# Kernel optimization log

Measured on AMD Instinct MI355X. Metric: run time of the kernel, lower is better.

The kernel has to match this reference:

```python
import jax, jax.numpy as jnp
import numpy as np

D_MODEL = 256
NHEAD = 8
HEAD_DIM = D_MODEL // NHEAD
NLAYERS = 8
LAYER_NAMES = ('self', 'cross', 'self', 'cross', 'self', 'cross', 'self', 'cross')
LN_EPS = 1e-5
ATTN_EPS = 1e-6


def _layernorm(x, g, b):
    mu = jnp.mean(x, axis=-1, keepdims=True)
    var = jnp.mean(jnp.square(x - mu), axis=-1, keepdims=True)
    return (x - mu) * jax.lax.rsqrt(var + LN_EPS) * g + b


def _encoder_layer(x, source, Wq, Wk, Wv, Wm, W1, W2, g1, b1, g2, b2):
    # x: [N, L, C], source: [N, S, C]; weights stored [in, out] so y = x @ W
    bs, L, C = x.shape
    S = source.shape[1]
    q = (x @ Wq).reshape(bs, L, NHEAD, HEAD_DIM)
    k = (source @ Wk).reshape(bs, S, NHEAD, HEAD_DIM)
    v = (source @ Wv).reshape(bs, S, NHEAD, HEAD_DIM)
    # LoFTR LinearAttention: feature map elu(x)+1, O(N d^2) kernelized attention
    Q = jax.nn.elu(q) + 1.0
    K = jax.nn.elu(k) + 1.0
    v_n = v / S  # normalize values by kv length for numerical stability
    KV = jnp.einsum('nshd,nshv->nhdv', K, v_n)            # [N,H,D,D]
    Z = 1.0 / (jnp.einsum('nlhd,nhd->nlh', Q, K.sum(axis=1)) + ATTN_EPS)
    msg = jnp.einsum('nlhd,nhdv,nlh->nlhv', Q, KV, Z) * S  # [N,L,H,D]
    msg = msg.reshape(bs, L, C) @ Wm
    msg = _layernorm(msg, g1, b1)
    h = jnp.concatenate([x, msg], axis=-1)                 # [N,L,2C]
    h = jax.nn.relu(h @ W1) @ W2
    h = _layernorm(h, g2, b2)
    return x + h


def _transformer(feat0, feat1, Wq, Wk, Wv, Wm, W1, W2, g1, b1, g2, b2):
    for i, name in enumerate(LAYER_NAMES):
        p = (Wq[i], Wk[i], Wv[i], Wm[i], W1[i], W2[i], g1[i], b1[i], g2[i], b2[i])
        if name == 'self':
            feat0 = _encoder_layer(feat0, feat0, *p)
            feat1 = _encoder_layer(feat1, feat1, *p)
        else:  # cross
            new0 = _encoder_layer(feat0, feat1, *p)
            feat1 = _encoder_layer(feat1, feat0, *p)
            feat0 = new0
    return feat0, feat1


def setup_inputs() -> dict:
    key = jax.random.key(0)
    ks = jax.random.split(key, 8)
    N, L = 4, 4800
    feat0 = jax.random.normal(ks[0], (N, L, D_MODEL), jnp.float32)
    feat1 = jax.random.normal(ks[1], (N, L, D_MODEL), jnp.float32)
    xav = lambda k, fi, fo: jax.random.normal(k, (NLAYERS, fi, fo), jnp.float32) * float(np.sqrt(2.0 / (fi + fo)))
    Wq = xav(ks[2], D_MODEL, D_MODEL)
    Wk = xav(ks[3], D_MODEL, D_MODEL)
    Wv = xav(ks[4], D_MODEL, D_MODEL)
    Wm = xav(ks[5], D_MODEL, D_MODEL)
    W1 = xav(ks[6], 2 * D_MODEL, 2 * D_MODEL)
    W2 = xav(ks[7], 2 * D_MODEL, D_MODEL)
    g1 = jnp.ones((NLAYERS, D_MODEL), jnp.float32)
    b1 = jnp.zeros((NLAYERS, D_MODEL), jnp.float32)
    g2 = jnp.ones((NLAYERS, D_MODEL), jnp.float32)
    b2 = jnp.zeros((NLAYERS, D_MODEL), jnp.float32)
    return dict(feat0=feat0, feat1=feat1, Wq=Wq, Wk=Wk, Wv=Wv, Wm=Wm,
                W1=W1, W2=W2, g1=g1, b1=b1, g2=g2, b2=b2)


def reference(feat0, feat1, Wq, Wk, Wv, Wm, W1, W2, g1, b1, g2, b2):
    return _transformer(feat0, feat1, Wq, Wk, Wv, Wm, W1, W2, g1, b1, g2, b2)
```

## Files before the change

kernel.cpp:

```cpp
#include <hip/hip_runtime.h>
#include <math.h>

#define RTOT 19200
#define RALL 38400
#define CDIM 256
#define SLEN 4800
#define NB 8
#define NHEAD 8
#define HDIM 32
#define SEG 25
#define SCHUNK 192

typedef __attribute__((ext_vector_type(8))) short short8v;
typedef __attribute__((ext_vector_type(4))) float f32x4;

__device__ __forceinline__ ushort f2b(float f) {
    unsigned u = __float_as_uint(f);
    unsigned r = (u + 0x7FFFu + ((u >> 16) & 1u)) >> 16;
    return (ushort)r;
}
__device__ __forceinline__ float b2f(ushort u) {
    return __uint_as_float(((unsigned)u) << 16);
}

template<int ACT> __device__ __forceinline__ float actf(float v) {
    if (ACT == 1) return v > 0.0f ? v + 1.0f : __expf(v);
    if (ACT == 2) return v > 0.0f ? v : 0.0f;
    return v;
}

__device__ __forceinline__ void gload16(const void* g, void* l) {
    __builtin_amdgcn_global_load_lds((const __attribute__((address_space(1))) void*)g,
                                     (__attribute__((address_space(3))) void*)l, 16, 0, 0);
}

template<int ACT, bool CONCAT, int OMODE>
__global__ __launch_bounds__(256) void gemm_bf16(
    const ushort* __restrict__ A, const ushort* __restrict__ A2, int lda,
    const ushort* __restrict__ Bt,
    ushort* __restrict__ O0, ushort* __restrict__ O1, ushort* __restrict__ O2,
    int N, int K)
{
    __shared__ __align__(16) ushort As[128 * 32];
    __shared__ __align__(16) ushort Bs[128 * 32];
    const int t = threadIdx.x;
    const int wave = t >> 6, lane = t & 63;
    const int bm = blockIdx.y * 128, bn = blockIdx.x * 128;
    const int wr = wave >> 1, wc = wave & 1;
    const int lr = lane & 15, lk = (lane >> 4) * 8;

    const int srow = t >> 2;
    const int sgrp = ((t & 3) * 8) ^ ((srow & 3) * 8);
    const ushort* bAr = A + (size_t)(bm + srow) * lda + sgrp;
    const ushort* bA2r = CONCAT ? (A2 + (size_t)(bm + srow) * lda + sgrp) : (const ushort*)0;
    const ushort* bBr = Bt + (size_t)(bn + srow) * K + sgrp;
    char* ldsA = (char*)As + wave * 1024;
    char* ldsB = (char*)Bs + wave * 1024;
    const size_t a64 = (size_t)64 * lda;
    const size_t b64 = (size_t)64 * K;

    const f32x4 z4 = {0.f, 0.f, 0.f, 0.f};
    f32x4 acc[4][4];
    #pragma unroll
    for (int m = 0; m < 4; ++m)
        #pragma unroll
        for (int n = 0; n < 4; ++n) acc[m][n] = z4;

    for (int k0 = 0; k0 < K; k0 += 32) {
        const ushort* ga;
        if (CONCAT) ga = (k0 < 256) ? (bAr + k0) : (bA2r + (k0 - 256));
        else        ga = bAr + k0;
        gload16(ga, ldsA);
        gload16(ga + a64, ldsA + 4096);
        gload16(bBr + k0, ldsB);
        gload16(bBr + k0 + b64, ldsB + 4096);
        __syncthreads();

        short8v af[4], bfr[4];
        #pragma unroll
        for (int m = 0; m < 4; ++m) {
            const int r = wr * 64 + m * 16 + lr;
            af[m] = *(const short8v*)&As[r * 32 + (lk ^ ((r & 3) * 8))];
        }
        #pragma unroll
        for (int n = 0; n < 4; ++n) {
            const int r = wc * 64 + n * 16 + lr;
            bfr[n] = *(const short8v*)&Bs[r * 32 + (lk ^ ((r & 3) * 8))];
        }
        #pragma unroll
        for (int m = 0; m < 4; ++m)
            #pragma unroll
            for (int n = 0; n < 4; ++n)
                acc[m][n] = __builtin_amdgcn_mfma_f32_16x16x32_bf16(af[m], bfr[n], acc[m][n], 0, 0, 0);
        __syncthreads();
    }

    const int orow = bm + wr * 64 + (lane >> 4) * 4;
    const int ocol = bn + wc * 64 + lr;
    #pragma unroll
    for (int m = 0; m < 4; ++m)
        #pragma unroll
        for (int n = 0; n < 4; ++n)
            #pragma unroll
            for (int j = 0; j < 4; ++j) {
                const float v = acc[m][n][j];
                const size_t row = (size_t)(orow + m * 16 + j);
                const int col = ocol + n * 16;
                if (OMODE == 0) {
                    O0[row * N + col] = f2b(actf<ACT>(v));
                } else {
                    const int seg = col >> 8, c = col & 255;
                    ushort* dst = seg == 0 ? O0 : (seg == 1 ? O1 : O2);
                    dst[row * 256 + c] = f2b(seg < 2 ? actf<1>(v) : v);
                }
            }
}

__global__ __launch_bounds__(256) void gemm_ln32(
    const ushort* __restrict__ A, int lda,
    const ushort* __restrict__ Bt,
    const float* __restrict__ g, const float* __restrict__ bb,
    const float* __restrict__ rx0, const float* __restrict__ rx1,
    float* __restrict__ outf, ushort* __restrict__ outb, int K)
{
    __shared__ __align__(16) ushort As[32 * 32];
    __shared__ __align__(16) ushort Bs[256 * 32];
    __shared__ float red[2][4][32];
    const int t = threadIdx.x;
    const int wave = t >> 6, lane = t & 63;
    const int bm = blockIdx.x * 32;
    const int lr = lane & 15, kg = lane >> 4, lk = kg * 8;

    const int srow = t >> 2;
    const int sg = ((t & 3) * 8) ^ ((srow & 3) * 8);
    const ushort* aP = A + (size_t)(bm + srow) * lda + sg;
    const ushort* bP = Bt + (size_t)srow * K + sg;
    char* ldsA = (char*)As + wave * 1024;
    char* ldsB = (char*)Bs + wave * 1024;
    const size_t b64 = (size_t)64 * K;

    const f32x4 z4 = {0.f, 0.f, 0.f, 0.f};
    f32x4 acc[2][4];
    #pragma unroll
    for (int m = 0; m < 2; ++m)
        #pragma unroll
        for (int n = 0; n < 4; ++n) acc[m][n] = z4;

    for (int k0 = 0; k0 < K; k0 += 32) {
        if (srow < 32) gload16(aP + k0, ldsA);
        gload16(bP + k0, ldsB);
        gload16(bP + k0 + b64, ldsB + 4096);
        gload16(bP + k0 + 2 * b64, ldsB + 8192);
        gload16(bP + k0 + 3 * b64, ldsB + 12288);
        __syncthreads();

        short8v af[2], bfr[4];
        #pragma unroll
        for (int m = 0; m < 2; ++m) {
            const int r = m * 16 + lr;
            af[m] = *(const short8v*)&As[r * 32 + (lk ^ ((r & 3) * 8))];
        }
        #pragma unroll
        for (int n = 0; n < 4; ++n) {
            const int r = wave * 64 + n * 16 + lr;
            bfr[n] = *(const short8v*)&Bs[r * 32 + (lk ^ ((r & 3) * 8))];
        }
        #pragma unroll
        for (int m = 0; m < 2; ++m)
            #pragma unroll
            for (int n = 0; n < 4; ++n)
                acc[m][n] = __builtin_amdgcn_mfma_f32_16x16x32_bf16(af[m], bfr[n], acc[m][n], 0, 0, 0);
        __syncthreads();
    }

    #pragma unroll
    for (int m = 0; m < 2; ++m)
        #pragma unroll
        for (int j = 0; j < 4; ++j) {
            float s = 0.f, q = 0.f;
            #pragma unroll
            for (int n = 0; n < 4; ++n) { const float v = acc[m][n][j]; s += v; q += v * v; }
            #pragma unroll
            for (int mk = 1; mk < 16; mk <<= 1) { s += __shfl_xor(s, mk); q += __shfl_xor(q, mk); }
            if (lr == 0) {
                red[0][wave][m * 16 + kg * 4 + j] = s;
                red[1][wave][m * 16 + kg * 4 + j] = q;
            }
        }
    __syncthreads();

    float gv[4], bv[4];
    #pragma unroll
    for (int n = 0; n < 4; ++n) {
        const int col = wave * 64 + n * 16 + lr;
        gv[n] = g[col]; bv[n] = bb[col];
    }
    const float* rxb = (bm < RTOT) ? rx0 + (size_t)bm * CDIM : rx1 + (size_t)(bm - RTOT) * CDIM;

    #pragma unroll
    for (int m = 0; m < 2; ++m)
        #pragma unroll
        for (int j = 0; j < 4; ++j) {
            const int row = m * 16 + kg * 4 + j;
            const float tot = red[0][0][row] + red[0][1][row] + red[0][2][row] + red[0][3][row];
            const float tq  = red[1][0][row] + red[1][1][row] + red[1][2][row] + red[1][3][row];
            const float mu = tot * (1.0f / 256.0f);
            const float var = tq * (1.0f / 256.0f) - mu * mu;
            const float inv = rsqrtf(var + 1e-5f);
            const size_t go = (size_t)(bm + row) * CDIM;
            #pragma unroll
            for (int n = 0; n < 4; ++n) {
                const int col = wave * 64 + n * 16 + lr;
                float val = (acc[m][n][j] - mu) * inv * gv[n] + bv[n];
                val += rxb[(size_t)row * CDIM + col];
                outf[go + col] = val;
                outb[go + col] = f2b(val);
            }
        }
}

__global__ __launch_bounds__(256) void attn_wm_ln(
    const ushort* __restrict__ Qb, const ushort* __restrict__ KVbT,
    const ushort* __restrict__ Ksb, const ushort* __restrict__ WmT,
    const float* __restrict__ g, const float* __restrict__ bb,
    ushort* __restrict__ mln, int xorv)
{
    __shared__ __align__(16) ushort Ms[32 * 256];
    __shared__ __align__(16) ushort Bs[256 * 32];
    __shared__ float red[2][4][32];
    const int t = threadIdx.x, wave = t >> 6, lane = t & 63;
    const int bm = blockIdx.x * 32;
    const int n = bm / SLEN, src = n ^ xorv;
    const int lr = lane & 15, kg = lane >> 4, lk = kg * 8;
    const f32x4 z4 = {0.f, 0.f, 0.f, 0.f};

    if (wave < 2) {
        const int rw = wave * 16;
        const size_t qrow = ((size_t)bm + rw + lr) * CDIM;
        char* mb = (char*)Ms;
        #pragma unroll
        for (int h = 0; h < NHEAD; ++h) {
            const short8v af = *(const short8v*)&Qb[qrow + h * 32 + kg * 8];
            const ushort* bbp = KVbT + ((size_t)(src * NHEAD + h)) * 1024;
            const short8v b0 = *(const short8v*)&bbp[lr * 32 + kg * 8];
            const short8v b1 = *(const short8v*)&bbp[(16 + lr) * 32 + kg * 8];
            const short8v bz = *(const short8v*)&Ksb[((size_t)(src * NHEAD + h)) * 512 + lr * 32 + kg * 8];
            f32x4 a0 = __builtin_amdgcn_mfma_f32_16x16x32_bf16(af, b0, z4, 0, 0, 0);
            f32x4 a1 = __builtin_amdgcn_mfma_f32_16x16x32_bf16(af, b1, z4, 0, 0, 0);
            f32x4 az = __builtin_amdgcn_mfma_f32_16x16x32_bf16(af, bz, z4, 0, 0, 0);
            #pragma unroll
            for (int j = 0; j < 4; ++j) {
                const float zj = __shfl(az[j], lane & 48);
                const float rz = 1.0f / (zj + 1e-6f);
                const int orow = rw + kg * 4 + j;
                const int swz = (orow & 7) << 4;
                *(ushort*)(mb + ((orow * 512 + (h * 32 + lr) * 2) ^ swz)) = f2b(a0[j] * rz);
                *(ushort*)(mb + ((orow * 512 + (h * 32 + 16 + lr) * 2) ^ swz)) = f2b(a1[j] * rz);
            }
        }
    }
    __syncthreads();

    const int srow = t >> 2;
    const int sg = ((t & 3) * 8) ^ ((srow & 3) * 8);
    const ushort* bP = WmT + (size_t)srow * 256 + sg;
    char* ldsB = (char*)Bs + wave * 1024;

    f32x4 acc[2][4];
    #pragma unroll
    for (int m = 0; m < 2; ++m)
        #pragma unroll
        for (int nn = 0; nn < 4; ++nn) acc[m][nn] = z4;

    for (int k0 = 0; k0 < 256; k0 += 32) {
        gload16(bP + k0, ldsB);
        gload16(bP + k0 + 64 * 256, ldsB + 4096);
        gload16(bP + k0 + 128 * 256, ldsB + 8192);
        gload16(bP + k0 + 192 * 256, ldsB + 12288);
        __syncthreads();

        short8v af[2], bfr[4];
        #pragma unroll
        for (int m = 0; m < 2; ++m) {
            const int r = m * 16 + lr;
            af[m] = *(const short8v*)((char*)Ms + ((r * 512 + k0 * 2 + kg * 16) ^ ((r & 7) << 4)));
        }
        #pragma unroll
        for (int nn = 0; nn < 4; ++nn) {
            const int r = wave * 64 + nn * 16 + lr;
            bfr[nn] = *(const short8v*)&Bs[r * 32 + (lk ^ ((r & 3) * 8))];
        }
        #pragma unroll
        for (int m = 0; m < 2; ++m)
            #pragma unroll
            for (int nn = 0; nn < 4; ++nn)
                acc[m][nn] = __builtin_amdgcn_mfma_f32_16x16x32_bf16(af[m], bfr[nn], acc[m][nn], 0, 0, 0);
        __syncthreads();
    }

    #pragma unroll
    for (int m = 0; m < 2; ++m)
        #pragma unroll
        for (int j = 0; j < 4; ++j) {
            float s = 0.f, q = 0.f;
            #pragma unroll
            for (int nn = 0; nn < 4; ++nn) { const float v = acc[m][nn][j]; s += v; q += v * v; }
            #pragma unroll
            for (int mk = 1; mk < 16; mk <<= 1) { s += __shfl_xor(s, mk); q += __shfl_xor(q, mk); }
            if (lr == 0) {
                red[0][wave][m * 16 + kg * 4 + j] = s;
                red[1][wave][m * 16 + kg * 4 + j] = q;
            }
        }
    __syncthreads();

    float gv[4], bv[4];
    #pragma unroll
    for (int nn = 0; nn < 4; ++nn) {
        const int col = wave * 64 + nn * 16 + lr;
        gv[nn] = g[col]; bv[nn] = bb[col];
    }
    #pragma unroll
    for (int m = 0; m < 2; ++m)
        #pragma unroll
        for (int j = 0; j < 4; ++j) {
            const int row = m * 16 + kg * 4 + j;
            const float tot = red[0][0][row] + red[0][1][row] + red[0][2][row] + red[0][3][row];
            const float tq  = red[1][0][row] + red[1][1][row] + red[1][2][row] + red[1][3][row];
            const float mu = tot * (1.0f / 256.0f);
            const float var = tq * (1.0f / 256.0f) - mu * mu;
            const float inv = rsqrtf(var + 1e-5f);
            const size_t go = (size_t)(bm + row) * CDIM;
            #pragma unroll
            for (int nn = 0; nn < 4; ++nn) {
                const int col = wave * 64 + nn * 16 + lr;
                mln[go + col] = f2b((acc[m][nn][j] - mu) * inv * gv[nn] + bv[nn]);
            }
        }
}

__global__ __launch_bounds__(256) void wconv_t(
    const float* __restrict__ src, ushort* __restrict__ dst, int R, int C, size_t dstride)
{
    __shared__ float tile[32][33];
    const int l = blockIdx.z;
    const int r0 = blockIdx.y * 32, c0 = blockIdx.x * 32;
    const int tx = threadIdx.x & 31, ty = threadIdx.x >> 5;
    const float* s = src + (size_t)l * R * C;
    ushort* d = dst + (size_t)l * dstride;
    for (int i = ty; i < 32; i += 8) tile[i][tx] = s[(size_t)(r0 + i) * C + c0 + tx];
    __syncthreads();
    for (int i = ty; i < 32; i += 8) d[(size_t)(c0 + i) * R + r0 + tx] = f2b(tile[tx][i]);
}

__global__ __launch_bounds__(256) void kv_part_k(
    const ushort* __restrict__ Kb, const ushort* __restrict__ Vb,
    float* __restrict__ KVp, float* __restrict__ Ksp)
{
    const int blk = blockIdx.x;
    const int seg = blk % SEG;
    const int h = (blk / SEG) % NHEAD;
    const int n = blk / (SEG * NHEAD);
    const int s0 = seg * SCHUNK;
    __shared__ float Ks[16][32];
    __shared__ float Vs[16][32];
    const int t = threadIdx.x;
    const int rr = t >> 4, c2 = (t & 15) * 2;
    const int d = t >> 3, v0 = (t & 7) * 4;
    float a0 = 0, a1 = 0, a2 = 0, a3 = 0, ksum = 0;
    for (int c = 0; c < SCHUNK; c += 16) {
        const size_t off = ((size_t)(n * SLEN + s0 + c + rr)) * CDIM + h * HDIM + c2;
        const ushort2 ku = *(const ushort2*)&Kb[off];
        const ushort2 vu = *(const ushort2*)&Vb[off];
        Ks[rr][c2] = b2f(ku.x); Ks[rr][c2 + 1] = b2f(ku.y);
        Vs[rr][c2] = b2f(vu.x); Vs[rr][c2 + 1] = b2f(vu.y);
        __syncthreads();
        #pragma unroll
        for (int q = 0; q < 16; ++q) {
            const float kd = Ks[q][d];
            a0 += kd * Vs[q][v0 + 0];
            a1 += kd * Vs[q][v0 + 1];
            a2 += kd * Vs[q][v0 + 2];
            a3 += kd * Vs[q][v0 + 3];
        }
        if (t < 32) {
            #pragma unroll
            for (int q = 0; q < 16; ++q) ksum += Ks[q][t];
        }
        __syncthreads();
    }
    float* kvp = KVp + ((size_t)((n * NHEAD + h) * SEG + seg)) * 1024;
    kvp[t * 4 + 0] = a0;
    kvp[t * 4 + 1] = a1;
    kvp[t * 4 + 2] = a2;
    kvp[t * 4 + 3] = a3;
    if (t < 32) Ksp[((size_t)((n * NHEAD + h) * SEG + seg)) * 32 + t] = ksum;
}

__global__ __launch_bounds__(256) void kv_reduce_k(
    const float* __restrict__ KVp, const float* __restrict__ Ksp,
    ushort* __restrict__ KVbT, ushort* __restrict__ Ksb)
{
    const int nh = blockIdx.x;
    const int t = threadIdx.x;
    #pragma unroll
    for (int i = 0; i < 4; ++i) {
        const int idx = t * 4 + i;
        const int v = idx >> 5, d = idx & 31;
        float s = 0;
        for (int seg = 0; seg < SEG; ++seg)
            s += KVp[((size_t)(nh * SEG + seg)) * 1024 + d * 32 + v];
        KVbT[(size_t)nh * 1024 + idx] = f2b(s);
    }
    #pragma unroll
    for (int i = 0; i < 2; ++i) {
        const int idx = t * 2 + i;
        const int c = idx >> 5, d = idx & 31;
        float s = 0;
        if (c == 0)
            for (int seg = 0; seg < SEG; ++seg)
                s += Ksp[((size_t)(nh * SEG + seg)) * 32 + d];
        Ksb[(size_t)nh * 512 + idx] = f2b(s);
    }
}

__global__ __launch_bounds__(256) void cvt_in_k(const float* __restrict__ src, ushort* __restrict__ dst) {
    const size_t i = ((size_t)blockIdx.x * 256 + threadIdx.x) * 4;
    const float4 v = *(const float4*)&src[i];
    ushort4 ob = make_ushort4(f2b(v.x), f2b(v.y), f2b(v.z), f2b(v.w));
    *(ushort4*)&dst[i] = ob;
}

struct Ws {
    float *xf, *KVp, *Ksp;
    ushort *xb, *Qb, *Kb, *Vb, *h1b, *KVbT, *Ksb;
    ushort *WqkvT, *WmT, *W1T, *W2T;
};

static void layer_pass(const float* rx0, const float* rx1, float* destf, int xorv,
                       const ushort* WqkvT, const ushort* WmT,
                       const ushort* W1T, const ushort* W2T,
                       const float* g1, const float* b1,
                       const float* g2, const float* b2,
                       const Ws& w, hipStream_t stream)
{
    const dim3 blk(256);
    gemm_bf16<0, false, 1><<<dim3(6, RALL / 128), blk, 0, stream>>>(
        w.xb, nullptr, 256, WqkvT, w.Qb, w.Kb, w.Vb, 768, 256);
    kv_part_k<<<dim3(NB * NHEAD * SEG), blk, 0, stream>>>(w.Kb, w.Vb, w.KVp, w.Ksp);
    kv_reduce_k<<<dim3(NB * NHEAD), blk, 0, stream>>>(w.KVp, w.Ksp, w.KVbT, w.Ksb);
    attn_wm_ln<<<dim3(RALL / 32), blk, 0, stream>>>(
        w.Qb, w.KVbT, w.Ksb, WmT, g1, b1, w.Kb, xorv);
    gemm_bf16<2, true, 0><<<dim3(4, RALL / 128), blk, 0, stream>>>(
        w.xb, w.Kb, 256, W1T, w.h1b, nullptr, nullptr, 512, 512);
    gemm_ln32<<<dim3(RALL / 32), blk, 0, stream>>>(
        w.h1b, 512, W2T, g2, b2, rx0, rx1, destf, w.xb, 512);
}

extern "C" void kernel_launch(void* const* d_in, const int* in_sizes, int n_in,
                              void* d_out, int out_size, void* d_ws, size_t ws_size,
                              hipStream_t stream) {
    (void)in_sizes; (void)n_in; (void)out_size; (void)ws_size;
    const float* f0in = (const float*)d_in[0];
    const float* f1in = (const float*)d_in[1];
    const float* WqA = (const float*)d_in[2];
    const float* WkA = (const float*)d_in[3];
    const float* WvA = (const float*)d_in[4];
    const float* WmA = (const float*)d_in[5];
    const float* W1A = (const float*)d_in[6];
    const float* W2A = (const float*)d_in[7];
    const float* g1A = (const float*)d_in[8];
    const float* b1A = (const float*)d_in[9];
    const float* g2A = (const float*)d_in[10];
    const float* b2A = (const float*)d_in[11];

    float* outf = (float*)d_out;
    const size_t RC = (size_t)RTOT * CDIM;
    const size_t RAC = (size_t)RALL * CDIM;

    float* wsf = (float*)d_ws;
    Ws w;
    w.xf  = wsf;
    w.KVp = w.xf + RAC;
    w.Ksp = w.KVp + (size_t)64 * SEG * 1024;
    ushort* p = (ushort*)(w.Ksp + 64 * SEG * 32);
    w.xb = p;   p += RAC;
    w.Qb = p;   p += RAC;
    w.Kb = p;   p += RAC;
    w.Vb = p;   p += RAC;
    w.h1b = p;  p += (size_t)RALL * 512;
    w.KVbT = p; p += 64 * 1024;
    w.Ksb = p;  p += 64 * 512;
    w.WqkvT = p; p += (size_t)8 * 768 * 256;
    w.WmT = p;  p += (size_t)8 * 256 * 256;
    w.W1T = p;  p += (size_t)8 * 512 * 512;
    w.W2T = p;  p += (size_t)8 * 512 * 256;

    const dim3 blk(256);
    wconv_t<<<dim3(8, 8, 8), blk, 0, stream>>>(WqA, w.WqkvT,             256, 256, 768 * 256);
    wconv_t<<<dim3(8, 8, 8), blk, 0, stream>>>(WkA, w.WqkvT + 256 * 256, 256, 256, 768 * 256);
    wconv_t<<<dim3(8, 8, 8), blk, 0, stream>>>(WvA, w.WqkvT + 512 * 256, 256, 256, 768 * 256);
    wconv_t<<<dim3(8, 8, 8), blk, 0, stream>>>(WmA, w.WmT, 256, 256, 65536);
    wconv_t<<<dim3(16, 16, 8), blk, 0, stream>>>(W1A, w.W1T, 512, 512, 262144);
    wconv_t<<<dim3(8, 16, 8), blk, 0, stream>>>(W2A, w.W2T, 512, 256, 131072);

    cvt_in_k<<<dim3(RC / 1024), blk, 0, stream>>>(f0in, w.xb);
    cvt_in_k<<<dim3(RC / 1024), blk, 0, stream>>>(f1in, w.xb + RC);

    for (int l = 0; l < 8; ++l) {
        const int xorv = (l & 1) ? 4 : 0;
        const float* rx0 = (l == 0) ? f0in : w.xf;
        const float* rx1 = (l == 0) ? f1in : w.xf + RC;
        float* destf = (l == 7) ? outf : w.xf;
        layer_pass(rx0, rx1, destf, xorv,
                   w.WqkvT + (size_t)l * 768 * 256,
                   w.WmT + (size_t)l * 65536,
                   w.W1T + (size_t)l * 262144,
                   w.W2T + (size_t)l * 131072,
                   g1A + l * 256, b1A + l * 256, g2A + l * 256, b2A + l * 256,
                   w, stream);
    }
}
```

Before: 1.501 ms.

## Fuse MLP GEMMs with LayerNorm and double-buffer weight tiles

Replaces the separate W1 GEMM (with concat and ReLU) and the W2+LayerNorm kernel with a single mlp_ln kernel. It keeps the concatenated 32x512 input tile and each 128-wide chunk of the hidden activation in LDS, so the h1b intermediate is never written to or read back from global memory. The QKV GEMM and the Wm-projection kernel now double-buffer their LDS weight tiles so global loads overlap the MFMA work. The attention-message step is also spread across all four waves. In exchange, every 32-row block streams the full W1 and W2 weights, and the larger LDS footprint may lower occupancy.

```diff
diff --git a/kernel.cpp b/kernel.cpp
--- a/kernel.cpp
+++ b/kernel.cpp
@@ -7,7 +7,6 @@
 #define SLEN 4800
 #define NB 8
 #define NHEAD 8
-#define HDIM 32
 #define SEG 25
 #define SCHUNK 192
 
@@ -23,26 +22,19 @@
     return __uint_as_float(((unsigned)u) << 16);
 }
 
-template<int ACT> __device__ __forceinline__ float actf(float v) {
-    if (ACT == 1) return v > 0.0f ? v + 1.0f : __expf(v);
-    if (ACT == 2) return v > 0.0f ? v : 0.0f;
-    return v;
-}
+__device__ __forceinline__ float elu1(float v) { return v > 0.0f ? v + 1.0f : __expf(v); }
 
 __device__ __forceinline__ void gload16(const void* g, void* l) {
     __builtin_amdgcn_global_load_lds((const __attribute__((address_space(1))) void*)g,
                                      (__attribute__((address_space(3))) void*)l, 16, 0, 0);
 }
 
-template<int ACT, bool CONCAT, int OMODE>
-__global__ __launch_bounds__(256) void gemm_bf16(
-    const ushort* __restrict__ A, const ushort* __restrict__ A2, int lda,
-    const ushort* __restrict__ Bt,
-    ushort* __restrict__ O0, ushort* __restrict__ O1, ushort* __restrict__ O2,
-    int N, int K)
-{
-    __shared__ __align__(16) ushort As[128 * 32];
-    __shared__ __align__(16) ushort Bs[128 * 32];
+__global__ __launch_bounds__(256) void qkv_gemm(
+    const ushort* __restrict__ A, const ushort* __restrict__ Bt,
+    ushort* __restrict__ Oq, ushort* __restrict__ Ok, ushort* __restrict__ Ov)
+{
+    __shared__ __align__(16) ushort As[2][128 * 32];
+    __shared__ __align__(16) ushort Bs[2][128 * 32];
     const int t = threadIdx.x;
     const int wave = t >> 6, lane = t & 63;
     const int bm = blockIdx.y * 128, bn = blockIdx.x * 128;
@@ -51,13 +43,8 @@
 
     const int srow = t >> 2;
     const int sgrp = ((t & 3) * 8) ^ ((srow & 3) * 8);
-    const ushort* bAr = A + (size_t)(bm + srow) * lda + sgrp;
-    const ushort* bA2r = CONCAT ? (A2 + (size_t)(bm + srow) * lda + sgrp) : (const ushort*)0;
-    const ushort* bBr = Bt + (size_t)(bn + srow) * K + sgrp;
-    char* ldsA = (char*)As + wave * 1024;
-    char* ldsB = (char*)Bs + wave * 1024;
-    const size_t a64 = (size_t)64 * lda;
-    const size_t b64 = (size_t)64 * K;
+    const ushort* bAr = A + (size_t)(bm + srow) * 256 + sgrp;
+    const ushort* bBr = Bt + (size_t)(bn + srow) * 256 + sgrp;
 
     const f32x4 z4 = {0.f, 0.f, 0.f, 0.f};
     f32x4 acc[4][4];
@@ -66,26 +53,30 @@
         #pragma unroll
         for (int n = 0; n < 4; ++n) acc[m][n] = z4;
 
-    for (int k0 = 0; k0 < K; k0 += 32) {
-        const ushort* ga;
-        if (CONCAT) ga = (k0 < 256) ? (bAr + k0) : (bA2r + (k0 - 256));
-        else        ga = bAr + k0;
-        gload16(ga, ldsA);
-        gload16(ga + a64, ldsA + 4096);
-        gload16(bBr + k0, ldsB);
-        gload16(bBr + k0 + b64, ldsB + 4096);
-        __syncthreads();
-
+    auto stage = [&](int k0, int b) {
+        char* la = (char*)As[b] + wave * 1024;
+        char* lb = (char*)Bs[b] + wave * 1024;
+        gload16(bAr + k0, la);
+        gload16(bAr + k0 + 64 * 256, la + 4096);
+        gload16(bBr + k0, lb);
+        gload16(bBr + k0 + 64 * 256, lb + 4096);
+    };
+
+    stage(0, 0);
+    __syncthreads();
+    int cur = 0;
+    for (int k0 = 0; k0 < 256; k0 += 32) {
+        if (k0 + 32 < 256) stage(k0 + 32, cur ^ 1);
         short8v af[4], bfr[4];
         #pragma unroll
         for (int m = 0; m < 4; ++m) {
             const int r = wr * 64 + m * 16 + lr;
-            af[m] = *(const short8v*)&As[r * 32 + (lk ^ ((r & 3) * 8))];
+            af[m] = *(const short8v*)&As[cur][r * 32 + (lk ^ ((r & 3) * 8))];
         }
         #pragma unroll
         for (int n = 0; n < 4; ++n) {
             const int r = wc * 64 + n * 16 + lr;
-            bfr[n] = *(const short8v*)&Bs[r * 32 + (lk ^ ((r & 3) * 8))];
+            bfr[n] = *(const short8v*)&Bs[cur][r * 32 + (lk ^ ((r & 3) * 8))];
         }
         #pragma unroll
         for (int m = 0; m < 4; ++m)
@@ -93,6 +84,7 @@
             for (int n = 0; n < 4; ++n)
                 acc[m][n] = __builtin_amdgcn_mfma_f32_16x16x32_bf16(af[m], bfr[n], acc[m][n], 0, 0, 0);
         __syncthreads();
+        cur ^= 1;
     }
 
     const int orow = bm + wr * 64 + (lane >> 4) * 4;
@@ -106,71 +98,92 @@
                 const float v = acc[m][n][j];
                 const size_t row = (size_t)(orow + m * 16 + j);
                 const int col = ocol + n * 16;
-                if (OMODE == 0) {
-                    O0[row * N + col] = f2b(actf<ACT>(v));
-                } else {
-                    const int seg = col >> 8, c = col & 255;
-                    ushort* dst = seg == 0 ? O0 : (seg == 1 ? O1 : O2);
-                    dst[row * 256 + c] = f2b(seg < 2 ? actf<1>(v) : v);
-                }
-            }
-}
-
-__global__ __launch_bounds__(256) void gemm_ln32(
-    const ushort* __restrict__ A, int lda,
-    const ushort* __restrict__ Bt,
+                const int seg = col >> 8, c = col & 255;
+                ushort* dst = seg == 0 ? Oq : (seg == 1 ? Ok : Ov);
+                dst[row * 256 + c] = f2b(seg < 2 ? elu1(v) : v);
+            }
+}
+
+__global__ __launch_bounds__(256) void attn_wm_ln(
+    const ushort* __restrict__ Qb, const ushort* __restrict__ KVbT,
+    const ushort* __restrict__ Ksb, const ushort* __restrict__ WmT,
     const float* __restrict__ g, const float* __restrict__ bb,
-    const float* __restrict__ rx0, const float* __restrict__ rx1,
-    float* __restrict__ outf, ushort* __restrict__ outb, int K)
-{
-    __shared__ __align__(16) ushort As[32 * 32];
-    __shared__ __align__(16) ushort Bs[256 * 32];
+    ushort* __restrict__ mln, int xorv)
+{
+    __shared__ __align__(16) ushort Ms[32 * 256];
+    __shared__ __align__(16) ushort Bs[2][256 * 32];
     __shared__ float red[2][4][32];
-    const int t = threadIdx.x;
-    const int wave = t >> 6, lane = t & 63;
+    const int t = threadIdx.x, wave = t >> 6, lane = t & 63;
     const int bm = blockIdx.x * 32;
+    const int n = bm / SLEN, src = n ^ xorv;
     const int lr = lane & 15, kg = lane >> 4, lk = kg * 8;
+    const f32x4 z4 = {0.f, 0.f, 0.f, 0.f};
 
     const int srow = t >> 2;
     const int sg = ((t & 3) * 8) ^ ((srow & 3) * 8);
-    const ushort* aP = A + (size_t)(bm + srow) * lda + sg;
-    const ushort* bP = Bt + (size_t)srow * K + sg;
-    char* ldsA = (char*)As + wave * 1024;
-    char* ldsB = (char*)Bs + wave * 1024;
-    const size_t b64 = (size_t)64 * K;
-
-    const f32x4 z4 = {0.f, 0.f, 0.f, 0.f};
+    const ushort* bP = WmT + (size_t)srow * 256 + sg;
+    auto stageB = [&](int k0, int b) {
+        char* lb = (char*)Bs[b] + wave * 1024;
+        gload16(bP + k0, lb);
+        gload16(bP + k0 + 64 * 256, lb + 4096);
+        gload16(bP + k0 + 128 * 256, lb + 8192);
+        gload16(bP + k0 + 192 * 256, lb + 12288);
+    };
+    stageB(0, 0);
+
+    {
+        const int rw = (wave & 1) * 16;
+        const size_t qrow = ((size_t)bm + rw + lr) * CDIM;
+        char* mb = (char*)Ms;
+        for (int h = (wave >> 1); h < NHEAD; h += 2) {
+            const short8v af = *(const short8v*)&Qb[qrow + h * 32 + kg * 8];
+            const ushort* bbp = KVbT + ((size_t)(src * NHEAD + h)) * 1024;
+            const short8v b0 = *(const short8v*)&bbp[lr * 32 + kg * 8];
+            const short8v b1 = *(const short8v*)&bbp[(16 + lr) * 32 + kg * 8];
+            const short8v bz = *(const short8v*)&Ksb[((size_t)(src * NHEAD + h)) * 512 + lr * 32 + kg * 8];
+            f32x4 a0 = __builtin_amdgcn_mfma_f32_16x16x32_bf16(af, b0, z4, 0, 0, 0);
+            f32x4 a1 = __builtin_amdgcn_mfma_f32_16x16x32_bf16(af, b1, z4, 0, 0, 0);
+            f32x4 az = __builtin_amdgcn_mfma_f32_16x16x32_bf16(af, bz, z4, 0, 0, 0);
+            #pragma unroll
+            for (int j = 0; j < 4; ++j) {
+                const float zj = __shfl(az[j], lane & 48);
+                const float rz = 1.0f / (zj + 1e-6f);
+                const int orow = rw + kg * 4 + j;
+                const int swz = (orow & 7) << 4;
+                *(ushort*)(mb + ((orow * 512 + (h * 32 + lr) * 2) ^ swz)) = f2b(a0[j] * rz);
+                *(ushort*)(mb + ((orow * 512 + (h * 32 + 16 + lr) * 2) ^ swz)) = f2b(a1[j] * rz);
+            }
+        }
+    }
+    __syncthreads();
+
     f32x4 acc[2][4];
     #pragma unroll
     for (int m = 0; m < 2; ++m)
         #pragma unroll
-        for (int n = 0; n < 4; ++n) acc[m][n] = z4;
-
-    for (int k0 = 0; k0 < K; k0 += 32) {
-        if (srow < 32) gload16(aP + k0, ldsA);
-        gload16(bP + k0, ldsB);
-        gload16(bP + k0 + b64, ldsB + 4096);
-        gload16(bP + k0 + 2 * b64, ldsB + 8192);
-        gload16(bP + k0 + 3 * b64, ldsB + 12288);
-        __syncthreads();
-
+        for (int nn = 0; nn < 4; ++nn) acc[m][nn] = z4;
+
+    int cur = 0;
+    for (int k0 = 0; k0 < 256; k0 += 32) {
+        if (k0 + 32 < 256) stageB(k0 + 32, cur ^ 1);
         short8v af[2], bfr[4];
         #pragma unroll
         for (int m = 0; m < 2; ++m) {
             const int r = m * 16 + lr;
-            af[m] = *(const short8v*)&As[r * 32 + (lk ^ ((r & 3) * 8))];
-        }
-        #pragma unroll
-        for (int n = 0; n < 4; ++n) {
-            const int r = wave * 64 + n * 16 + lr;
-            bfr[n] = *(const short8v*)&Bs[r * 32 + (lk ^ ((r & 3) * 8))];
+            af[m] = *(const short8v*)((char*)Ms + ((r * 512 + k0 * 2 + kg * 16) ^ ((r & 7) << 4)));
+        }
+        #pragma unroll
+        for (int nn = 0; nn < 4; ++nn) {
+            const int r = wave * 64 + nn * 16 + lr;
+            bfr[nn] = *(const short8v*)&Bs[cur][r * 32 + (lk ^ ((r & 3) * 8))];
         }
         #pragma unroll
         for (int m = 0; m < 2; ++m)
             #pragma unroll
-            for (int n = 0; n < 4; ++n)
-                acc[m][n] = __builtin_amdgcn_mfma_f32_16x16x32_bf16(af[m], bfr[n], acc[m][n], 0, 0, 0);
+            for (int nn = 0; nn < 4; ++nn)
+                acc[m][nn] = __builtin_amdgcn_mfma_f32_16x16x32_bf16(af[m], bfr[nn], acc[m][nn], 0, 0, 0);
         __syncthreads();
+        cur ^= 1;
     }
 
     #pragma unroll
@@ -179,7 +192,7 @@
         for (int j = 0; j < 4; ++j) {
             float s = 0.f, q = 0.f;
             #pragma unroll
-            for (int n = 0; n < 4; ++n) { const float v = acc[m][n][j]; s += v; q += v * v; }
+            for (int nn = 0; nn < 4; ++nn) { const float v = acc[m][nn][j]; s += v; q += v * v; }
             #pragma unroll
             for (int mk = 1; mk < 16; mk <<= 1) { s += __shfl_xor(s, mk); q += __shfl_xor(q, mk); }
             if (lr == 0) {
@@ -191,12 +204,10 @@
 
     float gv[4], bv[4];
     #pragma unroll
-    for (int n = 0; n < 4; ++n) {
-        const int col = wave * 64 + n * 16 + lr;
-        gv[n] = g[col]; bv[n] = bb[col];
-    }
-    const float* rxb = (bm < RTOT) ? rx0 + (size_t)bm * CDIM : rx1 + (size_t)(bm - RTOT) * CDIM;
-
+    for (int nn = 0; nn < 4; ++nn) {
+        const int col = wave * 64 + nn * 16 + lr;
+        gv[nn] = g[col]; bv[nn] = bb[col];
+    }
     #pragma unroll
     for (int m = 0; m < 2; ++m)
         #pragma unroll
@@ -209,93 +220,141 @@
             const float inv = rsqrtf(var + 1e-5f);
             const size_t go = (size_t)(bm + row) * CDIM;
             #pragma unroll
-            for (int n = 0; n < 4; ++n) {
-                const int col = wave * 64 + n * 16 + lr;
-                float val = (acc[m][n][j] - mu) * inv * gv[n] + bv[n];
-                val += rxb[(size_t)row * CDIM + col];
-                outf[go + col] = val;
-                outb[go + col] = f2b(val);
-            }
-        }
-}
-
-__global__ __launch_bounds__(256) void attn_wm_ln(
-    const ushort* __restrict__ Qb, const ushort* __restrict__ KVbT,
-    const ushort* __restrict__ Ksb, const ushort* __restrict__ WmT,
+            for (int nn = 0; nn < 4; ++nn) {
+                const int col = wave * 64 + nn * 16 + lr;
+                mln[go + col] = f2b((acc[m][nn][j] - mu) * inv * gv[nn] + bv[nn]);
+            }
+        }
+}
+
+__global__ __launch_bounds__(256) void mlp_ln(
+    const ushort* __restrict__ xb, const ushort* __restrict__ mlnSrc,
+    const ushort* __restrict__ W1T, const ushort* __restrict__ W2T,
     const float* __restrict__ g, const float* __restrict__ bb,
-    ushort* __restrict__ mln, int xorv)
-{
-    __shared__ __align__(16) ushort Ms[32 * 256];
-    __shared__ __align__(16) ushort Bs[256 * 32];
+    const float* __restrict__ rx0, const float* __restrict__ rx1,
+    float* __restrict__ outf, ushort* __restrict__ outb)
+{
+    __shared__ __align__(16) ushort A512[32 * 512];
+    __shared__ __align__(16) ushort Bs[2][256 * 32];
+    __shared__ __align__(16) ushort H1[32 * 128];
     __shared__ float red[2][4][32];
     const int t = threadIdx.x, wave = t >> 6, lane = t & 63;
     const int bm = blockIdx.x * 32;
-    const int n = bm / SLEN, src = n ^ xorv;
     const int lr = lane & 15, kg = lane >> 4, lk = kg * 8;
     const f32x4 z4 = {0.f, 0.f, 0.f, 0.f};
 
-    if (wave < 2) {
-        const int rw = wave * 16;
-        const size_t qrow = ((size_t)bm + rw + lr) * CDIM;
-        char* mb = (char*)Ms;
-        #pragma unroll
-        for (int h = 0; h < NHEAD; ++h) {
-            const short8v af = *(const short8v*)&Qb[qrow + h * 32 + kg * 8];
-            const ushort* bbp = KVbT + ((size_t)(src * NHEAD + h)) * 1024;
-            const short8v b0 = *(const short8v*)&bbp[lr * 32 + kg * 8];
-            const short8v b1 = *(const short8v*)&bbp[(16 + lr) * 32 + kg * 8];
-            const short8v bz = *(const short8v*)&Ksb[((size_t)(src * NHEAD + h)) * 512 + lr * 32 + kg * 8];
-            f32x4 a0 = __builtin_amdgcn_mfma_f32_16x16x32_bf16(af, b0, z4, 0, 0, 0);
-            f32x4 a1 = __builtin_amdgcn_mfma_f32_16x16x32_bf16(af, b1, z4, 0, 0, 0);
-            f32x4 az = __builtin_amdgcn_mfma_f32_16x16x32_bf16(af, bz, z4, 0, 0, 0);
-            #pragma unroll
-            for (int j = 0; j < 4; ++j) {
-                const float zj = __shfl(az[j], lane & 48);
-                const float rz = 1.0f / (zj + 1e-6f);
-                const int orow = rw + kg * 4 + j;
-                const int swz = (orow & 7) << 4;
-                *(ushort*)(mb + ((orow * 512 + (h * 32 + lr) * 2) ^ swz)) = f2b(a0[j] * rz);
-                *(ushort*)(mb + ((orow * 512 + (h * 32 + 16 + lr) * 2) ^ swz)) = f2b(a1[j] * rz);
-            }
-        }
-    }
-    __syncthreads();
+    {
+        const ushort* mln2 = mlnSrc - 256;
+        #pragma unroll
+        for (int i = 0; i < 8; ++i) {
+            const int row = i * 4 + wave;
+            const int gl = lane ^ (row & 7);
+            const ushort* s = (gl < 32) ? (xb + (size_t)(bm + row) * 256 + gl * 8)
+                                        : (mln2 + (size_t)(bm + row) * 256 + gl * 8);
+            gload16(s, (char*)A512 + row * 1024);
+        }
+    }
 
     const int srow = t >> 2;
     const int sg = ((t & 3) * 8) ^ ((srow & 3) * 8);
-    const ushort* bP = WmT + (size_t)srow * 256 + sg;
-    char* ldsB = (char*)Bs + wave * 1024;
-
-    f32x4 acc[2][4];
+    auto stageIdx = [&](int idx, int b) {
+        char* lb = (char*)Bs[b] + wave * 1024;
+        const int c = idx / 12, s = idx % 12;
+        if (s < 8) {
+            const ushort* p = W1T + (size_t)(c * 128 + srow) * 512 + s * 64 + sg;
+            gload16(p, lb);
+            gload16(p + (size_t)64 * 512, lb + 4096);
+            gload16(p + 32, lb + 8192);
+            gload16(p + (size_t)64 * 512 + 32, lb + 12288);
+        } else {
+            const ushort* p = W2T + (size_t)srow * 512 + c * 128 + (s - 8) * 32 + sg;
+            gload16(p, lb);
+            gload16(p + (size_t)64 * 512, lb + 4096);
+            gload16(p + (size_t)128 * 512, lb + 8192);
+            gload16(p + (size_t)192 * 512, lb + 12288);
+        }
+    };
+
+    f32x4 acc2[2][4];
     #pragma unroll
     for (int m = 0; m < 2; ++m)
         #pragma unroll
-        for (int nn = 0; nn < 4; ++nn) acc[m][nn] = z4;
-
-    for (int k0 = 0; k0 < 256; k0 += 32) {
-        gload16(bP + k0, ldsB);
-        gload16(bP + k0 + 64 * 256, ldsB + 4096);
-        gload16(bP + k0 + 128 * 256, ldsB + 8192);
-        gload16(bP + k0 + 192 * 256, ldsB + 12288);
+        for (int nn = 0; nn < 4; ++nn) acc2[m][nn] = z4;
+
+    stageIdx(0, 0);
+    __syncthreads();
+    int cur = 0, sid = 0;
+
+    for (int c = 0; c < 4; ++c) {
+        f32x4 acc1[2][2];
+        #pragma unroll
+        for (int m = 0; m < 2; ++m)
+            #pragma unroll
+            for (int nn = 0; nn < 2; ++nn) acc1[m][nn] = z4;
+
+        for (int s = 0; s < 8; ++s) {
+            if (sid + 1 < 48) stageIdx(sid + 1, cur ^ 1);
+            #pragma unroll
+            for (int half = 0; half < 2; ++half) {
+                short8v af[2], bfr[2];
+                #pragma unroll
+                for (int m = 0; m < 2; ++m) {
+                    const int r = m * 16 + lr;
+                    const int q = s * 8 + half * 4 + kg;
+                    af[m] = *(const short8v*)((char*)A512 + r * 1024 + ((q ^ (r & 7)) << 4));
+                }
+                #pragma unroll
+                for (int nn = 0; nn < 2; ++nn) {
+                    const int r = wave * 32 + nn * 16 + lr;
+                    bfr[nn] = *(const short8v*)&Bs[cur][half * 4096 + r * 32 + (lk ^ ((r & 3) * 8))];
+                }
+                #pragma unroll
+                for (int m = 0; m < 2; ++m)
+                    #pragma unroll
+                    for (int nn = 0; nn < 2; ++nn)
+                        acc1[m][nn] = __builtin_amdgcn_mfma_f32_16x16x32_bf16(af[m], bfr[nn], acc1[m][nn], 0, 0, 0);
+            }
+            __syncthreads();
+            cur ^= 1; ++sid;
+        }
+
+        #pragma unroll
+        for (int m = 0; m < 2; ++m)
+            #pragma unroll
+            for (int nn = 0; nn < 2; ++nn)
+                #pragma unroll
+                for (int j = 0; j < 4; ++j) {
+                    const int row = m * 16 + kg * 4 + j;
+                    const int col = wave * 32 + nn * 16 + lr;
+                    const float v = acc1[m][nn][j];
+                    const int grp = col >> 3;
+                    *(ushort*)((char*)H1 + row * 256 + ((grp ^ (row & 7)) << 4) + (col & 7) * 2)
+                        = f2b(v > 0.f ? v : 0.f);
+                }
         __syncthreads();
 
-        short8v af[2], bfr[4];
-        #pragma unroll
-        for (int m = 0; m < 2; ++m) {
-            const int r = m * 16 + lr;
-            af[m] = *(const short8v*)((char*)Ms + ((r * 512 + k0 * 2 + kg * 16) ^ ((r & 7) << 4)));
-        }
-        #pragma unroll
-        for (int nn = 0; nn < 4; ++nn) {
-            const int r = wave * 64 + nn * 16 + lr;
-            bfr[nn] = *(const short8v*)&Bs[r * 32 + (lk ^ ((r & 3) * 8))];
-        }
-        #pragma unroll
-        for (int m = 0; m < 2; ++m)
-            #pragma unroll
-            for (int nn = 0; nn < 4; ++nn)
-                acc[m][nn] = __builtin_amdgcn_mfma_f32_16x16x32_bf16(af[m], bfr[nn], acc[m][nn], 0, 0, 0);
-        __syncthreads();
+        for (int s = 0; s < 4; ++s) {
+            if (sid + 1 < 48) stageIdx(sid + 1, cur ^ 1);
+            short8v af[2], bfr[4];
+            #pragma unroll
+            for (int m = 0; m < 2; ++m) {
+                const int r = m * 16 + lr;
+                const int q = s * 4 + kg;
+                af[m] = *(const short8v*)((char*)H1 + r * 256 + ((q ^ (r & 7)) << 4));
+            }
+            #pragma unroll
+            for (int nn = 0; nn < 4; ++nn) {
+                const int r = wave * 64 + nn * 16 + lr;
+                bfr[nn] = *(const short8v*)&Bs[cur][r * 32 + (lk ^ ((r & 3) * 8))];
+            }
+            #pragma unroll
+            for (int m = 0; m < 2; ++m)
+                #pragma unroll
+                for (int nn = 0; nn < 4; ++nn)
+                    acc2[m][nn] = __builtin_amdgcn_mfma_f32_16x16x32_bf16(af[m], bfr[nn], acc2[m][nn], 0, 0, 0);
+            __syncthreads();
+            cur ^= 1; ++sid;
+        }
     }
 
     #pragma unroll
@@ -304,7 +363,7 @@
         for (int j = 0; j < 4; ++j) {
             float s = 0.f, q = 0.f;
             #pragma unroll
-            for (int nn = 0; nn < 4; ++nn) { const float v = acc[m][nn][j]; s += v; q += v * v; }
+            for (int nn = 0; nn < 4; ++nn) { const float v = acc2[m][nn][j]; s += v; q += v * v; }
             #pragma unroll
             for (int mk = 1; mk < 16; mk <<= 1) { s += __shfl_xor(s, mk); q += __shfl_xor(q, mk); }
             if (lr == 0) {
@@ -320,6 +379,8 @@
         const int col = wave * 64 + nn * 16 + lr;
         gv[nn] = g[col]; bv[nn] = bb[col];
     }
+    const float* rxb = (bm < RTOT) ? rx0 + (size_t)bm * CDIM : rx1 + (size_t)(bm - RTOT) * CDIM;
+
     #pragma unroll
     for (int m = 0; m < 2; ++m)
         #pragma unroll
@@ -334,7 +395,10 @@
             #pragma unroll
             for (int nn = 0; nn < 4; ++nn) {
                 const int col = wave * 64 + nn * 16 + lr;
-                mln[go + col] = f2b((acc[m][nn][j] - mu) * inv * gv[nn] + bv[nn]);
+                float val = (acc2[m][nn][j] - mu) * inv * gv[nn] + bv[nn];
+                val += rxb[(size_t)row * CDIM + col];
+                outf[go + col] = val;
+                outb[go + col] = f2b(val);
             }
         }
 }
@@ -369,7 +433,7 @@
     const int d = t >> 3, v0 = (t & 7) * 4;
     float a0 = 0, a1 = 0, a2 = 0, a3 = 0, ksum = 0;
     for (int c = 0; c < SCHUNK; c += 16) {
-        const size_t off = ((size_t)(n * SLEN + s0 + c + rr)) * CDIM + h * HDIM + c2;
+        const size_t off = ((size_t)(n * SLEN + s0 + c + rr)) * CDIM + h * 32 + c2;
         const ushort2 ku = *(const ushort2*)&Kb[off];
         const ushort2 vu = *(const ushort2*)&Vb[off];
         Ks[rr][c2] = b2f(ku.x); Ks[rr][c2 + 1] = b2f(ku.y);
@@ -433,7 +497,7 @@
 
 struct Ws {
     float *xf, *KVp, *Ksp;
-    ushort *xb, *Qb, *Kb, *Vb, *h1b, *KVbT, *Ksb;
+    ushort *xb, *Qb, *Kb, *Vb, *KVbT, *Ksb;
     ushort *WqkvT, *WmT, *W1T, *W2T;
 };
 
@@ -445,16 +509,13 @@
                        const Ws& w, hipStream_t stream)
 {
     const dim3 blk(256);
-    gemm_bf16<0, false, 1><<<dim3(6, RALL / 128), blk, 0, stream>>>(
-        w.xb, nullptr, 256, WqkvT, w.Qb, w.Kb, w.Vb, 768, 256);
+    qkv_gemm<<<dim3(6, RALL / 128), blk, 0, stream>>>(w.xb, WqkvT, w.Qb, w.Kb, w.Vb);
     kv_part_k<<<dim3(NB * NHEAD * SEG), blk, 0, stream>>>(w.Kb, w.Vb, w.KVp, w.Ksp);
     kv_reduce_k<<<dim3(NB * NHEAD), blk, 0, stream>>>(w.KVp, w.Ksp, w.KVbT, w.Ksb);
     attn_wm_ln<<<dim3(RALL / 32), blk, 0, stream>>>(
         w.Qb, w.KVbT, w.Ksb, WmT, g1, b1, w.Kb, xorv);
-    gemm_bf16<2, true, 0><<<dim3(4, RALL / 128), blk, 0, stream>>>(
-        w.xb, w.Kb, 256, W1T, w.h1b, nullptr, nullptr, 512, 512);
-    gemm_ln32<<<dim3(RALL / 32), blk, 0, stream>>>(
-        w.h1b, 512, W2T, g2, b2, rx0, rx1, destf, w.xb, 512);
+    mlp_ln<<<dim3(RALL / 32), blk, 0, stream>>>(
+        w.xb, w.Kb, W1T, W2T, g2, b2, rx0, rx1, destf, w.xb);
 }
 
 extern "C" void kernel_launch(void* const* d_in, const int* in_sizes, int n_in,
@@ -488,7 +549,6 @@
     w.Qb = p;   p += RAC;
     w.Kb = p;   p += RAC;
     w.Vb = p;   p += RAC;
-    w.h1b = p;  p += (size_t)RALL * 512;
     w.KVbT = p; p += 64 * 1024;
     w.Ksb = p;  p += 64 * 512;
     w.WqkvT = p; p += (size_t)8 * 768 * 256;
```

Measured after the change: 1.648 ms. 1.1x slower.
